# Kernel optimization log

Hardware: AMD Instinct MI355X
Metric: run time of the kernel (lower is better)

Reference implementation:

```python
import jax, jax.numpy as jnp
import numpy as np

BATCH = 262144
MAX_PEP_LEN = 15     # max peptide length (rows of peptide encoding)
PEPTIDE_LEN = 9      # effective peptide length (canonical 9-mer key in mapping)
ALPHABET = 20        # amino acids
NUM_POCKETS = 34     # MHC pseudo-sequence pocket positions
FILTER = 9           # filter_size


def _pocket_mask():
    # Dense [P, L] 0/1 mask encoding peptide_length_to_pocket_to_peptide[9]:
    # pocket i aggregates peptide positions sorted({i % 9, 3 * (i % 3)}).
    M = np.zeros((NUM_POCKETS, MAX_PEP_LEN), dtype=np.float32)
    for i in range(NUM_POCKETS):
        for j in {i % PEPTIDE_LEN, 3 * (i % 3)}:
            M[i, j] = 1.0
    return jnp.asarray(M)


def setup_inputs() -> dict:
    key = jax.random.key(0)
    k1, k2, k3 = jax.random.split(key, 3)
    peptide_encoding = jax.random.normal(k1, (BATCH, MAX_PEP_LEN, ALPHABET), dtype=jnp.float32)
    pocket_encoding = jax.random.randint(k2, (BATCH, NUM_POCKETS), 0, ALPHABET)
    kernel = jax.random.normal(k3, (ALPHABET, FILTER), dtype=jnp.float32)
    return {"peptide_encoding": peptide_encoding,
            "pocket_encoding": pocket_encoding,
            "kernel": kernel}


def reference(peptide_encoding, pocket_encoding, kernel):
    # peptide_encoding: [B, L, A] float, pocket_encoding: [B, P] int, kernel: [A, F]
    M = _pocket_mask()  # [P, L]
    # np.convolve is linear in the peptide row and the filter is shared within a
    # pocket, so sum_j conv(pep[j], f_i) == conv(sum_j pep[j], f_i): aggregate first.
    agg = jnp.einsum('pl,bla->bpa', M, peptide_encoding)   # [B, P, A]
    filts = kernel[pocket_encoding]                        # [B, P, F] gather per pocket
    full_conv = jax.vmap(jax.vmap(lambda a, f: jnp.convolve(a, f, mode='full')))
    return full_conv(agg, filts)                           # [B, P, A + F - 1]
```

## Files before the change

kernel.cpp:

```cpp
#include <hip/hip_runtime.h>

#define BATCH      262144
#define PEP_ROWS   9
#define REC_STRIDE 300
#define A          20
#define P          34
#define F          9
#define OUTW       28
#define BPB        8
#define PAIRS      (BPB * P)
#define NTHREADS   256
#define OUT_PER_BLOCK (PAIRS * OUTW)

__global__ __launch_bounds__(NTHREADS, 4)
void pep_pocket_conv(const float* __restrict__ pep,
                     const int*   __restrict__ pocket,
                     const float* __restrict__ kern,
                     float*       __restrict__ out)
{
    __shared__ float sPep[BPB * PEP_ROWS * A];
    __shared__ float sK[A * F];
    __shared__ int   sIdx[PAIRS];
    __shared__ float sOut[PAIRS * (OUTW + 1)];

    const int t = threadIdx.x;
    const int b0 = blockIdx.x * BPB;
    const int pairBase = b0 * P;

    if (t < A * F) sK[t] = kern[t];

    for (int i = t; i < PAIRS; i += NTHREADS) sIdx[i] = pocket[pairBase + i];

    for (int i = t; i < BPB * 45; i += NTHREADS) {
        int lb = i / 45, v = i % 45;
        const float4 x = *(const float4*)(pep + (b0 + lb) * REC_STRIDE + v * 4);
        *(float4*)(&sPep[lb * (PEP_ROWS * A) + v * 4]) = x;
    }
    __syncthreads();

    for (int round = 0; round < 2; ++round) {
        const int pl = t + round * NTHREADS;
        if (pl < PAIRS) {
            const int lb = pl / P;
            const int p  = pl % P;
            const int r  = p % 9;
            const int j2 = 3 * (p % 3);
            const float* base = &sPep[lb * (PEP_ROWS * A)];

            float a[A];
            #pragma unroll
            for (int j = 0; j < A; ++j) {
                float v = base[r * A + j];
                if (j2 != r) v += base[j2 * A + j];
                a[j] = v;
            }

            const int c = sIdx[pl];
            float kf[F];
            #pragma unroll
            for (int f = 0; f < F; ++f) kf[f] = sK[c * F + f];

            float acc[OUTW];
            #pragma unroll
            for (int k = 0; k < OUTW; ++k) acc[k] = 0.f;
            #pragma unroll
            for (int f = 0; f < F; ++f) {
                #pragma unroll
                for (int j = 0; j < A; ++j)
                    acc[f + j] += kf[f] * a[j];
            }

            float* so = &sOut[pl * (OUTW + 1)];
            #pragma unroll
            for (int k = 0; k < OUTW; ++k) so[k] = acc[k];
        }
    }
    __syncthreads();

    const int outBase = pairBase * OUTW;
    for (int i = t; i < OUT_PER_BLOCK; i += NTHREADS) {
        const int pl = i / OUTW, k = i - pl * OUTW;
        out[outBase + i] = sOut[pl * (OUTW + 1) + k];
    }
}

extern "C" void kernel_launch(void* const* d_in, const int* in_sizes, int n_in,
                              void* d_out, int out_size, void* d_ws, size_t ws_size,
                              hipStream_t stream) {
    const float* pep    = (const float*)d_in[0];
    const int*   pocket = (const int*)d_in[1];
    const float* kern   = (const float*)d_in[2];
    float* out = (float*)d_out;

    const int grid = BATCH / BPB;
    pep_pocket_conv<<<grid, NTHREADS, 0, stream>>>(pep, pocket, kern, out);
}
```

Before: 1.252 ms.

## Map one thread per pair and write output directly with float4 stores

After: 1.257 ms. Within noise of the previous version (+0.4%).

```diff
diff --git a/kernel.cpp b/kernel.cpp
--- a/kernel.cpp
+++ b/kernel.cpp
@@ -1,16 +1,14 @@
 #include <hip/hip_runtime.h>
 
 #define BATCH      262144
-#define PEP_ROWS   9
 #define REC_STRIDE 300
 #define A          20
 #define P          34
 #define F          9
 #define OUTW       28
-#define BPB        8
-#define PAIRS      (BPB * P)
 #define NTHREADS   256
-#define OUT_PER_BLOCK (PAIRS * OUTW)
+#define NREC       9
+#define PEP_FLOATS 180
 
 __global__ __launch_bounds__(NTHREADS, 4)
 void pep_pocket_conv(const float* __restrict__ pep,
@@ -18,70 +16,66 @@
                      const float* __restrict__ kern,
                      float*       __restrict__ out)
 {
-    __shared__ float sPep[BPB * PEP_ROWS * A];
+    __shared__ float sPep[NREC * PEP_FLOATS];
     __shared__ float sK[A * F];
-    __shared__ int   sIdx[PAIRS];
-    __shared__ float sOut[PAIRS * (OUTW + 1)];
 
-    const int t = threadIdx.x;
-    const int b0 = blockIdx.x * BPB;
-    const int pairBase = b0 * P;
+    const int t  = threadIdx.x;
+    const int pl = blockIdx.x * NTHREADS + t;
+    const int b  = pl / P;
+    const int p  = pl - b * P;
+    const int bFirst = (blockIdx.x * NTHREADS) / P;
 
-    if (t < A * F) sK[t] = kern[t];
+    const int c = pocket[pl];
 
-    for (int i = t; i < PAIRS; i += NTHREADS) sIdx[i] = pocket[pairBase + i];
+    if (t < 45)
+        *(float4*)&sK[t * 4] = *(const float4*)(kern + t * 4);
 
-    for (int i = t; i < BPB * 45; i += NTHREADS) {
-        int lb = i / 45, v = i % 45;
-        const float4 x = *(const float4*)(pep + (b0 + lb) * REC_STRIDE + v * 4);
-        *(float4*)(&sPep[lb * (PEP_ROWS * A) + v * 4]) = x;
+    for (int i = t; i < NREC * 45; i += NTHREADS) {
+        const int rec = i / 45, v = i - rec * 45;
+        int bb = bFirst + rec;
+        if (bb >= BATCH) bb = BATCH - 1;
+        *(float4*)&sPep[i * 4] =
+            *(const float4*)(pep + (size_t)bb * REC_STRIDE + v * 4);
     }
     __syncthreads();
 
-    for (int round = 0; round < 2; ++round) {
-        const int pl = t + round * NTHREADS;
-        if (pl < PAIRS) {
-            const int lb = pl / P;
-            const int p  = pl % P;
-            const int r  = p % 9;
-            const int j2 = 3 * (p % 3);
-            const float* base = &sPep[lb * (PEP_ROWS * A)];
+    const int q  = p % F;
+    const int j2 = 3 * (p % 3);
+    const float sel = (j2 != q) ? 1.f : 0.f;
+    const float* base = &sPep[(b - bFirst) * PEP_FLOATS];
+    const float* rA = base + q  * A;
+    const float* rB = base + j2 * A;
 
-            float a[A];
-            #pragma unroll
-            for (int j = 0; j < A; ++j) {
-                float v = base[r * A + j];
-                if (j2 != r) v += base[j2 * A + j];
-                a[j] = v;
-            }
+    float a[A];
+    #pragma unroll
+    for (int v = 0; v < 5; ++v) {
+        const float4 x = *(const float4*)(rA + v * 4);
+        const float4 y = *(const float4*)(rB + v * 4);
+        a[v * 4 + 0] = x.x + sel * y.x;
+        a[v * 4 + 1] = x.y + sel * y.y;
+        a[v * 4 + 2] = x.z + sel * y.z;
+        a[v * 4 + 3] = x.w + sel * y.w;
+    }
 
-            const int c = sIdx[pl];
-            float kf[F];
-            #pragma unroll
-            for (int f = 0; f < F; ++f) kf[f] = sK[c * F + f];
+    float kf[F];
+    #pragma unroll
+    for (int f = 0; f < F; ++f) kf[f] = sK[c * F + f];
 
-            float acc[OUTW];
-            #pragma unroll
-            for (int k = 0; k < OUTW; ++k) acc[k] = 0.f;
-            #pragma unroll
-            for (int f = 0; f < F; ++f) {
-                #pragma unroll
-                for (int j = 0; j < A; ++j)
-                    acc[f + j] += kf[f] * a[j];
-            }
+    float acc[OUTW];
+    #pragma unroll
+    for (int k = 0; k < OUTW; ++k) acc[k] = 0.f;
+    #pragma unroll
+    for (int f = 0; f < F; ++f) {
+        #pragma unroll
+        for (int j = 0; j < A; ++j)
+            acc[f + j] += kf[f] * a[j];
+    }
 
-            float* so = &sOut[pl * (OUTW + 1)];
-            #pragma unroll
-            for (int k = 0; k < OUTW; ++k) so[k] = acc[k];
-        }
-    }
-    __syncthreads();
-
-    const int outBase = pairBase * OUTW;
-    for (int i = t; i < OUT_PER_BLOCK; i += NTHREADS) {
-        const int pl = i / OUTW, k = i - pl * OUTW;
-        out[outBase + i] = sOut[pl * (OUTW + 1) + k];
-    }
+    float4* op = (float4*)(out + (size_t)pl * OUTW);
+    #pragma unroll
+    for (int k = 0; k < 7; ++k)
+        op[k] = make_float4(acc[4 * k + 0], acc[4 * k + 1],
+                            acc[4 * k + 2], acc[4 * k + 3]);
 }
 
 extern "C" void kernel_launch(void* const* d_in, const int* in_sizes, int n_in,
@@ -92,6 +86,6 @@
     const float* kern   = (const float*)d_in[2];
     float* out = (float*)d_out;
 
-    const int grid = BATCH / BPB;
+    const int grid = (BATCH * P) / NTHREADS;
     pep_pocket_conv<<<grid, NTHREADS, 0, stream>>>(pep, pocket, kern, out);
 }
```
